# Kernel tuning notes

Measured on AMD Instinct MI355X. Metric: run time of the kernel, lower is better.

The kernel has to match this reference:

```python
import jax, jax.numpy as jnp
import numpy as np


def setup_inputs() -> dict:
    key = jax.random.key(0)
    kq, kk, kv = jax.random.split(key, 3)
    B, H, T, D = 2, 8, 8192, 64
    return {
        "Q": jax.random.normal(kq, (B, H, T, D), dtype=jnp.float32),
        "K": jax.random.normal(kk, (B, H, T, D), dtype=jnp.float32),
        "V": jax.random.normal(kv, (B, H, T, D), dtype=jnp.float32),
        "window_size": 512,
    }


def _gather_bands(x, nb, Wn):
    # x: [B,H,T,D] -> [B,H,nb,3*Wn,D], key blocks (i-1, i, i+1) per query block i
    B, H, T, D = x.shape
    xb = x.reshape(B, H, nb, Wn, D)
    xp = jnp.pad(xb, ((0, 0), (0, 0), (1, 1), (0, 0), (0, 0)))
    return jnp.concatenate([xp[:, :, i:i + nb] for i in range(3)], axis=3)


def reference(Q, K, V, window_size):
    # Sliding-window attention: softmax over keys with |q_idx - kv_idx| <= window_size,
    # computed block-sparsely (only the 3 neighboring key blocks per query block).
    B, H, T, D = Q.shape
    Wn = int(window_size)
    assert T % Wn == 0
    nb = T // Wn
    scale = 1.0 / (D ** 0.5)

    Qb = Q.reshape(B, H, nb, Wn, D)
    Kw = _gather_bands(K, nb, Wn)  # [B,H,nb,3W,D]
    Vw = _gather_bands(V, nb, Wn)

    # scores within the band: [B,H,nb,W,3W]
    s = jnp.einsum('bhnqd,bhnkd->bhnqk', Qb, Kw) * scale

    # exact band mask: global q = n*W + q_loc, global kv = (n-1)*W + k_loc
    q_loc = jnp.arange(Wn)[:, None]
    k_loc = jnp.arange(3 * Wn)[None, :]
    band = jnp.abs(q_loc + Wn - k_loc) <= Wn          # [W, 3W]
    kv_g = (jnp.arange(nb)[:, None] - 1) * Wn + jnp.arange(3 * Wn)[None, :]  # [nb, 3W]
    valid = (kv_g >= 0) & (kv_g < T)
    mask = band[None, :, :] & valid[:, None, :]        # [nb, W, 3W]

    s = jnp.where(mask[None, None], s, -jnp.inf)
    p = jax.nn.softmax(s, axis=-1)
    o = jnp.einsum('bhnqk,bhnkd->bhnqd', p, Vw)
    return o.reshape(B, H, T, D)
```

## Files before the change

### kernel.cpp

```cpp
#include <hip/hip_runtime.h>
#include <hip/hip_bf16.h>
#include <stdint.h>

typedef __attribute__((ext_vector_type(8))) short bf16x8;
typedef __attribute__((ext_vector_type(4))) short bf16x4;
typedef __attribute__((ext_vector_type(4))) float f32x4;

#define T_SEQ   8192
#define D_HEAD  64
#define NHEADS  16
#define WIN     512
#define BQ      128
#define BK      64
#define NTILES  (T_SEQ / BK)
#define LDSR    72
#define MASKVAL (-1.0e6f)

#define WS_NEEDED ((size_t)2 * NHEADS * T_SEQ * D_HEAD * 2)

#define MFMA16(a,b,c) __builtin_amdgcn_mfma_f32_16x16x16bf16_1k(a,b,c,0,0,0)

__device__ __forceinline__ short f2bf(float f) {
    union { float f; uint32_t u; } v; v.f = f;
    return (short)((v.u + 0x7FFFu + ((v.u >> 16) & 1u)) >> 16);
}

__device__ __forceinline__ uint32_t pkbf2(float lo, float hi) {
    union { __hip_bfloat162 h; uint32_t u; } c;
    c.h = __float22bfloat162_rn(make_float2(lo, hi));
    return c.u;
}

__global__ __launch_bounds__(256, 2)
void prep_kv(const float* __restrict__ Kg, const float* __restrict__ Vg,
             short* __restrict__ Kb, short* __restrict__ Vt)
{
    __shared__ float vt[64 * 65];
    const int tid  = threadIdx.x;
    const int tile = blockIdx.x & (NTILES - 1);
    const int head = blockIdx.x >> 7;
    const size_t off = ((size_t)head * T_SEQ + (size_t)tile * BK) * D_HEAD;

    const float* ks = Kg + off;
    short* kd = Kb + off;
    #pragma unroll
    for (int i = 0; i < 4; ++i) {
        int idx = tid + 256 * i;
        float4 v = *(const float4*)(ks + idx * 4);
        short4 h = { f2bf(v.x), f2bf(v.y), f2bf(v.z), f2bf(v.w) };
        *(short4*)(kd + idx * 4) = h;
    }

    const float* vs = Vg + off;
    #pragma unroll
    for (int i = 0; i < 4; ++i) {
        int idx = tid + 256 * i;
        int row = idx >> 4, c4 = (idx & 15) << 2;
        float4 v = *(const float4*)(vs + row * D_HEAD + c4);
        *(float4*)&vt[row * 65 + c4] = v;
    }
    __syncthreads();
    short* vd = Vt + ((size_t)head * NTILES + tile) * (BK * D_HEAD);
    {
        int d = tid >> 2, kq = (tid & 3) << 4;
        short out[16];
        #pragma unroll
        for (int j = 0; j < 16; ++j) out[j] = f2bf(vt[(kq + j) * 65 + d]);
        *(bf16x8*)(vd + d * BK + kq)     = *(bf16x8*)&out[0];
        *(bf16x8*)(vd + d * BK + kq + 8) = *(bf16x8*)&out[8];
    }
}

__global__ __launch_bounds__(256, 4)
void swa_fwd(const float* __restrict__ Qg, const short* __restrict__ Kb,
             const short* __restrict__ Vt, float* __restrict__ Og)
{
    __shared__ short Ks[BK * LDSR];
    __shared__ short Vs[D_HEAD * LDSR];

    const int tid  = threadIdx.x;
    const int wave = tid >> 6;
    const int lane = tid & 63;
    const int lcol = lane & 15;
    const int quad = lane >> 4;

    const int g    = blockIdx.x;
    const int head = (g >> 3) >> 3;
    const int qt   = ((g & 7) << 3) | ((g >> 3) & 7);
    const int q0   = qt * BQ;
    const int tq   = q0 >> 6;

    const float* Qp = Qg + (size_t)head * T_SEQ * D_HEAD;
    const short* Kp = Kb + (size_t)head * T_SEQ * D_HEAD;
    float*       Op = Og + (size_t)head * T_SEQ * D_HEAD;

    const float qscale = 0.125f * 1.44269504088896340736f;
    const int qrow_w = q0 + wave * 32;

    bf16x8 qf[2][2];
    #pragma unroll
    for (int mt = 0; mt < 2; ++mt) {
        const float* qptr = Qp + (size_t)(qrow_w + mt*16 + lcol) * D_HEAD + quad * 8;
        #pragma unroll
        for (int ks = 0; ks < 2; ++ks) {
            float4 a = *(const float4*)(qptr + ks*32);
            float4 b = *(const float4*)(qptr + ks*32 + 4);
            bf16x8 f;
            f[0]=f2bf(a.x*qscale); f[1]=f2bf(a.y*qscale); f[2]=f2bf(a.z*qscale); f[3]=f2bf(a.w*qscale);
            f[4]=f2bf(b.x*qscale); f[5]=f2bf(b.y*qscale); f[6]=f2bf(b.z*qscale); f[7]=f2bf(b.w*qscale);
            qf[mt][ks] = f;
        }
    }

    f32x4 oacc[2][4];
    float l_run[2];
    const f32x4 zero4 = {0.f, 0.f, 0.f, 0.f};
    #pragma unroll
    for (int mt = 0; mt < 2; ++mt) {
        l_run[mt] = 0.f;
        #pragma unroll
        for (int nt = 0; nt < 4; ++nt) oacc[mt][nt] = zero4;
    }

    int t0 = (q0 - WIN) >> 6;            if (t0 < 0) t0 = 0;
    int t1 = (q0 + BQ - 1 + WIN) >> 6;   if (t1 > NTILES - 1) t1 = NTILES - 1;

    for (int t = t0; t <= t1; ++t) {
        __syncthreads();
        {
            const short* ksrc = Kp + (size_t)t * BK * D_HEAD;
            const short* vsrc = Vt + ((size_t)head * NTILES + t) * (BK * D_HEAD);
            #pragma unroll
            for (int i = 0; i < 2; ++i) {
                int idx = tid + 256 * i;
                int row = idx >> 3, c = (idx & 7) << 3;
                *(bf16x8*)&Ks[row * LDSR + c] = *(const bf16x8*)(ksrc + idx * 8);
                *(bf16x8*)&Vs[row * LDSR + c] = *(const bf16x8*)(vsrc + idx * 8);
            }
        }
        __syncthreads();

        const bool edge = (t < tq - 6) || (t > tq + 7);

        #pragma unroll
        for (int h = 0; h < 2; ++h) {
            f32x4 sc[2][2];
            #pragma unroll
            for (int j = 0; j < 2; ++j) { sc[j][0] = zero4; sc[j][1] = zero4; }
            #pragma unroll
            for (int ks = 0; ks < 2; ++ks) {
                #pragma unroll
                for (int j = 0; j < 2; ++j) {
                    bf16x8 kf = *(const bf16x8*)&Ks[((2*h+j)*16 + lcol)*LDSR + ks*32 + quad*8];
                    sc[j][0] = __builtin_amdgcn_mfma_f32_16x16x32_bf16(kf, qf[0][ks], sc[j][0], 0,0,0);
                    sc[j][1] = __builtin_amdgcn_mfma_f32_16x16x32_bf16(kf, qf[1][ks], sc[j][1], 0,0,0);
                }
            }

            if (edge) {
                #pragma unroll
                for (int j = 0; j < 2; ++j) {
                    const int kg0 = t*BK + (2*h+j)*16 + quad*4;
                    #pragma unroll
                    for (int mt = 0; mt < 2; ++mt) {
                        const int qg = qrow_w + mt*16 + lcol;
                        #pragma unroll
                        for (int r = 0; r < 4; ++r) {
                            int dq = qg - (kg0 + r);
                            if (dq > WIN || dq < -WIN) sc[j][mt][r] = MASKVAL;
                        }
                    }
                }
            }

            #pragma unroll
            for (int j = 0; j < 2; ++j) {
                const int kt = 2*h + j;
                bf16x4 vf[4];
                #pragma unroll
                for (int nt = 0; nt < 4; ++nt)
                    vf[nt] = *(const bf16x4*)&Vs[(nt*16 + lcol)*LDSR + kt*16 + quad*4];
                #pragma unroll
                for (int mt = 0; mt < 2; ++mt) {
                    float p0 = exp2f(sc[j][mt][0]);
                    float p1 = exp2f(sc[j][mt][1]);
                    float p2 = exp2f(sc[j][mt][2]);
                    float p3 = exp2f(sc[j][mt][3]);
                    l_run[mt] += (p0 + p1) + (p2 + p3);
                    union { int2 i; bf16x4 v; } pf;
                    pf.i = make_int2((int)pkbf2(p0, p1), (int)pkbf2(p2, p3));
                    #pragma unroll
                    for (int nt = 0; nt < 4; ++nt)
                        oacc[mt][nt] = MFMA16(vf[nt], pf.v, oacc[mt][nt]);
                }
            }
        }
    }

    #pragma unroll
    for (int mt = 0; mt < 2; ++mt) {
        float l = l_run[mt];
        l += __shfl_xor(l, 16, 64);
        l += __shfl_xor(l, 32, 64);
        float inv = 1.0f / l;
        const int qg = qrow_w + mt*16 + lcol;
        float* op = Op + (size_t)qg * D_HEAD + quad*4;
        #pragma unroll
        for (int nt = 0; nt < 4; ++nt) {
            float4 o = { oacc[mt][nt][0]*inv, oacc[mt][nt][1]*inv,
                         oacc[mt][nt][2]*inv, oacc[mt][nt][3]*inv };
            *(float4*)(op + nt*16) = o;
        }
    }
}

#define M_INIT  (-1.0e4f)
__global__ __launch_bounds__(256, 2)
void swa_fwd_fb(const float* __restrict__ Qg, const float* __restrict__ Kg,
                const float* __restrict__ Vg, float* __restrict__ Og)
{
    __shared__ short Ks[BK * LDSR];
    __shared__ short Vs[D_HEAD * LDSR];
    __shared__ short Ps[4 * 32 * LDSR];

    const int tid  = threadIdx.x;
    const int wave = tid >> 6;
    const int lane = tid & 63;
    const int lcol = lane & 15;
    const int quad = lane >> 4;

    const int g    = blockIdx.x;
    const int head = (g >> 3) >> 3;
    const int qt   = ((g & 7) << 3) | ((g >> 3) & 7);
    const int q0   = qt * BQ;

    const size_t base = (size_t)head * T_SEQ * D_HEAD;
    const float* Qp = Qg + base;
    const float* Kp = Kg + base;
    const float* Vp = Vg + base;
    float*       Op = Og + base;

    const float qscale = 0.125f * 1.44269504088896340736f;
    const int qrow_w = q0 + wave * 32;

    bf16x8 qf[2][2];
    #pragma unroll
    for (int mt = 0; mt < 2; ++mt) {
        const float* qptr = Qp + (size_t)(qrow_w + mt*16 + lcol) * D_HEAD + quad * 8;
        #pragma unroll
        for (int ks = 0; ks < 2; ++ks) {
            float4 a = *(const float4*)(qptr + ks*32);
            float4 b = *(const float4*)(qptr + ks*32 + 4);
            bf16x8 f;
            f[0]=f2bf(a.x*qscale); f[1]=f2bf(a.y*qscale); f[2]=f2bf(a.z*qscale); f[3]=f2bf(a.w*qscale);
            f[4]=f2bf(b.x*qscale); f[5]=f2bf(b.y*qscale); f[6]=f2bf(b.z*qscale); f[7]=f2bf(b.w*qscale);
            qf[mt][ks] = f;
        }
    }

    f32x4 oacc[2][4];
    float m_run[2][4], l_run[2][4];
    const f32x4 zero4 = {0.f, 0.f, 0.f, 0.f};
    #pragma unroll
    for (int mt = 0; mt < 2; ++mt) {
        #pragma unroll
        for (int r = 0; r < 4; ++r) { m_run[mt][r] = M_INIT; l_run[mt][r] = 0.f; }
        #pragma unroll
        for (int nt = 0; nt < 4; ++nt) oacc[mt][nt] = zero4;
    }

    int t0 = (q0 - WIN) >> 6;            if (t0 < 0) t0 = 0;
    int t1 = (q0 + BQ - 1 + WIN) >> 6;   if (t1 > NTILES - 1) t1 = NTILES - 1;

    for (int t = t0; t <= t1; ++t) {
        __syncthreads();
        {
            const float* src = Kp + (size_t)t * BK * D_HEAD;
            #pragma unroll
            for (int i = 0; i < 4; ++i) {
                int f4 = tid + 256*i;
                int row = f4 >> 4, c4 = (f4 & 15) << 2;
                float4 v = *(const float4*)(src + row*D_HEAD + c4);
                short4 h = { f2bf(v.x), f2bf(v.y), f2bf(v.z), f2bf(v.w) };
                *(short4*)&Ks[row*LDSR + c4] = h;
            }
            const float* vsrc = Vp + (size_t)t * BK * D_HEAD;
            int col = tid & 63, rb = (tid >> 6) << 2;
            #pragma unroll
            for (int i = 0; i < 4; ++i) {
                int r = rb + 16*i;
                short4 h = { f2bf(vsrc[(r+0)*D_HEAD + col]),
                             f2bf(vsrc[(r+1)*D_HEAD + col]),
                             f2bf(vsrc[(r+2)*D_HEAD + col]),
                             f2bf(vsrc[(r+3)*D_HEAD + col]) };
                *(short4*)&Vs[col*LDSR + r] = h;
            }
        }
        __syncthreads();

        f32x4 sc[2][4];
        #pragma unroll
        for (int mt = 0; mt < 2; ++mt)
            #pragma unroll
            for (int kt = 0; kt < 4; ++kt) sc[mt][kt] = zero4;
        #pragma unroll
        for (int kt = 0; kt < 4; ++kt) {
            #pragma unroll
            for (int ks = 0; ks < 2; ++ks) {
                bf16x8 kf = *(const bf16x8*)&Ks[(kt*16 + lcol)*LDSR + ks*32 + quad*8];
                sc[0][kt] = __builtin_amdgcn_mfma_f32_16x16x32_bf16(qf[0][ks], kf, sc[0][kt], 0,0,0);
                sc[1][kt] = __builtin_amdgcn_mfma_f32_16x16x32_bf16(qf[1][ks], kf, sc[1][kt], 0,0,0);
            }
        }

        const int kb = t * BK + lcol;
        #pragma unroll
        for (int mt = 0; mt < 2; ++mt) {
            const int qrow = qrow_w + mt*16 + quad*4;
            #pragma unroll
            for (int kt = 0; kt < 4; ++kt) {
                int kg = kb + kt*16;
                #pragma unroll
                for (int r = 0; r < 4; ++r) {
                    int dq = (qrow + r) - kg;
                    if (dq > WIN || dq < -WIN) sc[mt][kt][r] = MASKVAL;
                }
            }
            float tm[4], al[4], rs[4];
            #pragma unroll
            for (int r = 0; r < 4; ++r)
                tm[r] = fmaxf(fmaxf(sc[mt][0][r], sc[mt][1][r]), fmaxf(sc[mt][2][r], sc[mt][3][r]));
            #pragma unroll
            for (int off = 1; off < 16; off <<= 1)
                #pragma unroll
                for (int r = 0; r < 4; ++r)
                    tm[r] = fmaxf(tm[r], __shfl_xor(tm[r], off, 64));
            #pragma unroll
            for (int r = 0; r < 4; ++r) {
                float mn = fmaxf(m_run[mt][r], tm[r]);
                al[r] = exp2f(m_run[mt][r] - mn);
                m_run[mt][r] = mn;
                rs[r] = 0.f;
            }
            #pragma unroll
            for (int kt = 0; kt < 4; ++kt)
                #pragma unroll
                for (int r = 0; r < 4; ++r) {
                    float p = exp2f(sc[mt][kt][r] - m_run[mt][r]);
                    sc[mt][kt][r] = p;
                    rs[r] += p;
                }
            #pragma unroll
            for (int off = 1; off < 16; off <<= 1)
                #pragma unroll
                for (int r = 0; r < 4; ++r)
                    rs[r] += __shfl_xor(rs[r], off, 64);
            #pragma unroll
            for (int r = 0; r < 4; ++r)
                l_run[mt][r] = l_run[mt][r]*al[r] + rs[r];
            #pragma unroll
            for (int nt = 0; nt < 4; ++nt)
                #pragma unroll
                for (int r = 0; r < 4; ++r) oacc[mt][nt][r] *= al[r];
            short* pw = &Ps[(wave*32 + mt*16 + quad*4) * LDSR];
            #pragma unroll
            for (int kt = 0; kt < 4; ++kt)
                #pragma unroll
                for (int r = 0; r < 4; ++r)
                    pw[r*LDSR + kt*16 + lcol] = f2bf(sc[mt][kt][r]);
        }

        const short* pr = &Ps[wave*32*LDSR];
        #pragma unroll
        for (int ks = 0; ks < 2; ++ks) {
            bf16x8 pf0 = *(const bf16x8*)&pr[(lcol     )*LDSR + ks*32 + quad*8];
            bf16x8 pf1 = *(const bf16x8*)&pr[(16 + lcol)*LDSR + ks*32 + quad*8];
            #pragma unroll
            for (int nt = 0; nt < 4; ++nt) {
                bf16x8 vf = *(const bf16x8*)&Vs[(nt*16 + lcol)*LDSR + ks*32 + quad*8];
                oacc[0][nt] = __builtin_amdgcn_mfma_f32_16x16x32_bf16(pf0, vf, oacc[0][nt], 0,0,0);
                oacc[1][nt] = __builtin_amdgcn_mfma_f32_16x16x32_bf16(pf1, vf, oacc[1][nt], 0,0,0);
            }
        }
    }

    #pragma unroll
    for (int mt = 0; mt < 2; ++mt)
        #pragma unroll
        for (int r = 0; r < 4; ++r) {
            int row = qrow_w + mt*16 + quad*4 + r;
            float inv = 1.0f / l_run[mt][r];
            float* op = Op + (size_t)row * D_HEAD + lcol;
            #pragma unroll
            for (int nt = 0; nt < 4; ++nt)
                op[nt*16] = oacc[mt][nt][r] * inv;
        }
}

extern "C" void kernel_launch(void* const* d_in, const int* in_sizes, int n_in,
                              void* d_out, int out_size, void* d_ws, size_t ws_size,
                              hipStream_t stream)
{
    const float* Q = (const float*)d_in[0];
    const float* K = (const float*)d_in[1];
    const float* V = (const float*)d_in[2];
    float* O = (float*)d_out;

    if (ws_size >= WS_NEEDED) {
        short* Kb = (short*)d_ws;
        short* Vt = Kb + (size_t)NHEADS * T_SEQ * D_HEAD;
        prep_kv<<<dim3(NHEADS * NTILES), dim3(256), 0, stream>>>(K, V, Kb, Vt);
        swa_fwd<<<dim3(NHEADS * (T_SEQ / BQ)), dim3(256), 0, stream>>>(Q, Kb, Vt, O);
    } else {
        swa_fwd_fb<<<dim3(NHEADS * (T_SEQ / BQ)), dim3(256), 0, stream>>>(Q, K, V, O);
    }
}
```

Before: 199.5 us.

## Double-buffer fragment-ordered KV tiles with larger query blocks and wider MFMA

The prep kernel now writes K and transposed V for each tile in one buffer, already in MFMA fragment order, so tiles can be copied into LDS without padding and read with aligned vector loads. The main kernel doubles the query block to 256 rows, so each wave handles 64 queries and K/V reuse per load goes up. It prefetches the next tile into registers while computing on the current one, using a ping-pong LDS buffer with one barrier per tile. The P·V product now uses 16x16x32 MFMAs instead of 16x16x16, and a wave skips tiles outside its own window. The costs are higher register pressure (occupancy hint drops from 4 to 2 blocks per CU) and half as many blocks.

```diff
diff --git a/kernel.cpp b/kernel.cpp
--- a/kernel.cpp
+++ b/kernel.cpp
@@ -10,15 +10,16 @@
 #define D_HEAD  64
 #define NHEADS  16
 #define WIN     512
-#define BQ      128
+#define BQ      256
 #define BK      64
-#define NTILES  (T_SEQ / BK)
-#define LDSR    72
+#define NTILES  128
+#define NQT     32
+#define TILE_SH 8192
 #define MASKVAL (-1.0e6f)
 
-#define WS_NEEDED ((size_t)2 * NHEADS * T_SEQ * D_HEAD * 2)
-
-#define MFMA16(a,b,c) __builtin_amdgcn_mfma_f32_16x16x16bf16_1k(a,b,c,0,0,0)
+#define WS_NEEDED ((size_t)NHEADS * NTILES * TILE_SH * sizeof(short))
+
+#define MFMA32(a,b,c) __builtin_amdgcn_mfma_f32_16x16x32_bf16(a,b,c,0,0,0)
 
 __device__ __forceinline__ short f2bf(float f) {
     union { float f; uint32_t u; } v; v.f = f;
@@ -33,50 +34,58 @@
 
 __global__ __launch_bounds__(256, 2)
 void prep_kv(const float* __restrict__ Kg, const float* __restrict__ Vg,
-             short* __restrict__ Kb, short* __restrict__ Vt)
+             short* __restrict__ KVf)
 {
     __shared__ float vt[64 * 65];
     const int tid  = threadIdx.x;
     const int tile = blockIdx.x & (NTILES - 1);
     const int head = blockIdx.x >> 7;
     const size_t off = ((size_t)head * T_SEQ + (size_t)tile * BK) * D_HEAD;
-
-    const float* ks = Kg + off;
-    short* kd = Kb + off;
-    #pragma unroll
-    for (int i = 0; i < 4; ++i) {
-        int idx = tid + 256 * i;
-        float4 v = *(const float4*)(ks + idx * 4);
-        short4 h = { f2bf(v.x), f2bf(v.y), f2bf(v.z), f2bf(v.w) };
-        *(short4*)(kd + idx * 4) = h;
-    }
+    short* KV = KVf + ((size_t)head * NTILES + tile) * TILE_SH;
 
     const float* vs = Vg + off;
     #pragma unroll
     for (int i = 0; i < 4; ++i) {
         int idx = tid + 256 * i;
         int row = idx >> 4, c4 = (idx & 15) << 2;
-        float4 v = *(const float4*)(vs + row * D_HEAD + c4);
-        *(float4*)&vt[row * 65 + c4] = v;
-    }
+        *(float4*)&vt[row * 65 + c4] = *(const float4*)(vs + row * D_HEAD + c4);
+    }
+
+    const float* ksrc = Kg + off;
+    #pragma unroll
+    for (int i = 0; i < 2; ++i) {
+        int b = tid + 256 * i;
+        int quad = b & 3, key = (b >> 2) & 15, ks = (b >> 6) & 1, kc = b >> 7;
+        const float* src = ksrc + (kc * 16 + key) * D_HEAD + ks * 32 + quad * 8;
+        float4 a = *(const float4*)src;
+        float4 c = *(const float4*)(src + 4);
+        bf16x8 o;
+        o[0]=f2bf(a.x); o[1]=f2bf(a.y); o[2]=f2bf(a.z); o[3]=f2bf(a.w);
+        o[4]=f2bf(c.x); o[5]=f2bf(c.y); o[6]=f2bf(c.z); o[7]=f2bf(c.w);
+        *(bf16x8*)(KV + b * 8) = o;
+    }
+
     __syncthreads();
-    short* vd = Vt + ((size_t)head * NTILES + tile) * (BK * D_HEAD);
-    {
-        int d = tid >> 2, kq = (tid & 3) << 4;
-        short out[16];
-        #pragma unroll
-        for (int j = 0; j < 16; ++j) out[j] = f2bf(vt[(kq + j) * 65 + d]);
-        *(bf16x8*)(vd + d * BK + kq)     = *(bf16x8*)&out[0];
-        *(bf16x8*)(vd + d * BK + kq + 8) = *(bf16x8*)&out[8];
-    }
-}
-
-__global__ __launch_bounds__(256, 4)
-void swa_fwd(const float* __restrict__ Qg, const short* __restrict__ Kb,
-             const short* __restrict__ Vt, float* __restrict__ Og)
+
+    #pragma unroll
+    for (int i = 0; i < 2; ++i) {
+        int b = tid + 256 * i;
+        int quad = b & 3, dl = (b >> 2) & 15, nt = (b >> 6) & 3, h = b >> 8;
+        int col = nt * 16 + dl;
+        bf16x8 o;
+        #pragma unroll
+        for (int j = 0; j < 4; ++j) o[j]     = f2bf(vt[(h*32 +      quad*4 + j) * 65 + col]);
+        #pragma unroll
+        for (int j = 0; j < 4; ++j) o[4 + j] = f2bf(vt[(h*32 + 16 + quad*4 + j) * 65 + col]);
+        *(bf16x8*)(KV + 4096 + b * 8) = o;
+    }
+}
+
+__global__ __launch_bounds__(256, 2)
+void swa_fwd(const float* __restrict__ Qg, const short* __restrict__ KVf,
+             float* __restrict__ Og)
 {
-    __shared__ short Ks[BK * LDSR];
-    __shared__ short Vs[D_HEAD * LDSR];
+    __shared__ __align__(16) short Buf[2][TILE_SH];
 
     const int tid  = threadIdx.x;
     const int wave = tid >> 6;
@@ -85,21 +94,21 @@
     const int quad = lane >> 4;
 
     const int g    = blockIdx.x;
-    const int head = (g >> 3) >> 3;
-    const int qt   = ((g & 7) << 3) | ((g >> 3) & 7);
+    const int head = ((g & 7) << 1) | ((g >> 3) & 1);
+    const int qt   = g >> 4;
     const int q0   = qt * BQ;
-    const int tq   = q0 >> 6;
-
-    const float* Qp = Qg + (size_t)head * T_SEQ * D_HEAD;
-    const short* Kp = Kb + (size_t)head * T_SEQ * D_HEAD;
-    float*       Op = Og + (size_t)head * T_SEQ * D_HEAD;
+    const int tb   = qt * 4;
+
+    const float* Qp  = Qg  + (size_t)head * T_SEQ * D_HEAD;
+    float*       Op  = Og  + (size_t)head * T_SEQ * D_HEAD;
+    const short* KVh = KVf + (size_t)head * NTILES * TILE_SH;
 
     const float qscale = 0.125f * 1.44269504088896340736f;
-    const int qrow_w = q0 + wave * 32;
-
-    bf16x8 qf[2][2];
-    #pragma unroll
-    for (int mt = 0; mt < 2; ++mt) {
+    const int qrow_w = q0 + wave * 64;
+
+    bf16x8 qf[4][2];
+    #pragma unroll
+    for (int mt = 0; mt < 4; ++mt) {
         const float* qptr = Qp + (size_t)(qrow_w + mt*16 + lcol) * D_HEAD + quad * 8;
         #pragma unroll
         for (int ks = 0; ks < 2; ++ks) {
@@ -112,93 +121,108 @@
         }
     }
 
-    f32x4 oacc[2][4];
-    float l_run[2];
+    f32x4 oacc[4][4];
+    float l_run[4];
     const f32x4 zero4 = {0.f, 0.f, 0.f, 0.f};
     #pragma unroll
-    for (int mt = 0; mt < 2; ++mt) {
+    for (int mt = 0; mt < 4; ++mt) {
         l_run[mt] = 0.f;
         #pragma unroll
         for (int nt = 0; nt < 4; ++nt) oacc[mt][nt] = zero4;
     }
 
-    int t0 = (q0 - WIN) >> 6;            if (t0 < 0) t0 = 0;
-    int t1 = (q0 + BQ - 1 + WIN) >> 6;   if (t1 > NTILES - 1) t1 = NTILES - 1;
-
+    int t0 = tb - 8;  if (t0 < 0) t0 = 0;
+    int t1 = tb + 11; if (t1 > NTILES - 1) t1 = NTILES - 1;
+
+    {
+        const short* src = KVh + (size_t)t0 * TILE_SH + tid * 8;
+        #pragma unroll
+        for (int i = 0; i < 4; ++i)
+            *(bf16x8*)&Buf[0][tid*8 + i*2048] = *(const bf16x8*)(src + i*2048);
+    }
+    __syncthreads();
+
+    int cur = 0;
     for (int t = t0; t <= t1; ++t) {
-        __syncthreads();
-        {
-            const short* ksrc = Kp + (size_t)t * BK * D_HEAD;
-            const short* vsrc = Vt + ((size_t)head * NTILES + t) * (BK * D_HEAD);
-            #pragma unroll
-            for (int i = 0; i < 2; ++i) {
-                int idx = tid + 256 * i;
-                int row = idx >> 3, c = (idx & 7) << 3;
-                *(bf16x8*)&Ks[row * LDSR + c] = *(const bf16x8*)(ksrc + idx * 8);
-                *(bf16x8*)&Vs[row * LDSR + c] = *(const bf16x8*)(vsrc + idx * 8);
-            }
-        }
-        __syncthreads();
-
-        const bool edge = (t < tq - 6) || (t > tq + 7);
-
-        #pragma unroll
-        for (int h = 0; h < 2; ++h) {
-            f32x4 sc[2][2];
-            #pragma unroll
-            for (int j = 0; j < 2; ++j) { sc[j][0] = zero4; sc[j][1] = zero4; }
-            #pragma unroll
-            for (int ks = 0; ks < 2; ++ks) {
-                #pragma unroll
-                for (int j = 0; j < 2; ++j) {
-                    bf16x8 kf = *(const bf16x8*)&Ks[((2*h+j)*16 + lcol)*LDSR + ks*32 + quad*8];
-                    sc[j][0] = __builtin_amdgcn_mfma_f32_16x16x32_bf16(kf, qf[0][ks], sc[j][0], 0,0,0);
-                    sc[j][1] = __builtin_amdgcn_mfma_f32_16x16x32_bf16(kf, qf[1][ks], sc[j][1], 0,0,0);
-                }
-            }
-
-            if (edge) {
-                #pragma unroll
-                for (int j = 0; j < 2; ++j) {
-                    const int kg0 = t*BK + (2*h+j)*16 + quad*4;
+        bf16x8 pre[4];
+        const bool have = (t < t1);
+        if (have) {
+            const short* src = KVh + (size_t)(t + 1) * TILE_SH + tid * 8;
+            #pragma unroll
+            for (int i = 0; i < 4; ++i) pre[i] = *(const bf16x8*)(src + i*2048);
+        }
+
+        if (t*BK <= qrow_w + 63 + WIN && t*BK + 63 >= qrow_w - WIN) {
+            const short* Kl = Buf[cur];
+            const short* Vl = Buf[cur] + 4096;
+            const bool edge = (t < tb - 4) || (t > tb + 7);
+
+            #pragma unroll
+            for (int h = 0; h < 2; ++h) {
+                bf16x4 pq[2][4];
+                #pragma unroll
+                for (int jj = 0; jj < 2; ++jj) {
+                    const int kc = h*2 + jj;
+                    bf16x8 kf0 = *(const bf16x8*)&Kl[((kc*2 + 0)*64 + lcol*4 + quad) * 8];
+                    bf16x8 kf1 = *(const bf16x8*)&Kl[((kc*2 + 1)*64 + lcol*4 + quad) * 8];
+                    f32x4 sc[4];
                     #pragma unroll
-                    for (int mt = 0; mt < 2; ++mt) {
-                        const int qg = qrow_w + mt*16 + lcol;
+                    for (int mt = 0; mt < 4; ++mt) sc[mt] = zero4;
+                    #pragma unroll
+                    for (int mt = 0; mt < 4; ++mt) {
+                        sc[mt] = MFMA32(kf0, qf[mt][0], sc[mt]);
+                        sc[mt] = MFMA32(kf1, qf[mt][1], sc[mt]);
+                    }
+                    if (edge) {
+                        const int kg0 = t*BK + kc*16 + quad*4;
                         #pragma unroll
-                        for (int r = 0; r < 4; ++r) {
-                            int dq = qg - (kg0 + r);
-                            if (dq > WIN || dq < -WIN) sc[j][mt][r] = MASKVAL;
+                        for (int mt = 0; mt < 4; ++mt) {
+                            const int qg = qrow_w + mt*16 + lcol;
+                            #pragma unroll
+                            for (int r = 0; r < 4; ++r) {
+                                int dq = qg - (kg0 + r);
+                                if (dq > WIN || dq < -WIN) sc[mt][r] = MASKVAL;
+                            }
                         }
                     }
+                    #pragma unroll
+                    for (int mt = 0; mt < 4; ++mt) {
+                        float p0 = exp2f(sc[mt][0]), p1 = exp2f(sc[mt][1]);
+                        float p2 = exp2f(sc[mt][2]), p3 = exp2f(sc[mt][3]);
+                        l_run[mt] += (p0 + p1) + (p2 + p3);
+                        union { int2 i2; bf16x4 v; } u;
+                        u.i2 = make_int2((int)pkbf2(p0, p1), (int)pkbf2(p2, p3));
+                        pq[jj][mt] = u.v;
+                    }
                 }
-            }
-
-            #pragma unroll
-            for (int j = 0; j < 2; ++j) {
-                const int kt = 2*h + j;
-                bf16x4 vf[4];
-                #pragma unroll
-                for (int nt = 0; nt < 4; ++nt)
-                    vf[nt] = *(const bf16x4*)&Vs[(nt*16 + lcol)*LDSR + kt*16 + quad*4];
-                #pragma unroll
-                for (int mt = 0; mt < 2; ++mt) {
-                    float p0 = exp2f(sc[j][mt][0]);
-                    float p1 = exp2f(sc[j][mt][1]);
-                    float p2 = exp2f(sc[j][mt][2]);
-                    float p3 = exp2f(sc[j][mt][3]);
-                    l_run[mt] += (p0 + p1) + (p2 + p3);
-                    union { int2 i; bf16x4 v; } pf;
-                    pf.i = make_int2((int)pkbf2(p0, p1), (int)pkbf2(p2, p3));
+                bf16x8 pf[4];
+                #pragma unroll
+                for (int mt = 0; mt < 4; ++mt) {
+                    union { bf16x8 v; bf16x4 q[2]; } u;
+                    u.q[0] = pq[0][mt]; u.q[1] = pq[1][mt];
+                    pf[mt] = u.v;
+                }
+                #pragma unroll
+                for (int nt = 0; nt < 4; ++nt) {
+                    bf16x8 vf = *(const bf16x8*)&Vl[((h*4 + nt)*64 + lcol*4 + quad) * 8];
                     #pragma unroll
-                    for (int nt = 0; nt < 4; ++nt)
-                        oacc[mt][nt] = MFMA16(vf[nt], pf.v, oacc[mt][nt]);
+                    for (int mt = 0; mt < 4; ++mt)
+                        oacc[mt][nt] = MFMA32(vf, pf[mt], oacc[mt][nt]);
                 }
             }
         }
-    }
-
-    #pragma unroll
-    for (int mt = 0; mt < 2; ++mt) {
+
+        if (have) {
+            #pragma unroll
+            for (int i = 0; i < 4; ++i)
+                *(bf16x8*)&Buf[cur ^ 1][tid*8 + i*2048] = pre[i];
+        }
+        __syncthreads();
+        cur ^= 1;
+    }
+
+    #pragma unroll
+    for (int mt = 0; mt < 4; ++mt) {
         float l = l_run[mt];
         l += __shfl_xor(l, 16, 64);
         l += __shfl_xor(l, 32, 64);
@@ -214,6 +238,7 @@
     }
 }
 
+#define LDSR    72
 #define M_INIT  (-1.0e4f)
 __global__ __launch_bounds__(256, 2)
 void swa_fwd_fb(const float* __restrict__ Qg, const float* __restrict__ Kg,
@@ -232,7 +257,7 @@
     const int g    = blockIdx.x;
     const int head = (g >> 3) >> 3;
     const int qt   = ((g & 7) << 3) | ((g >> 3) & 7);
-    const int q0   = qt * BQ;
+    const int q0   = qt * 128;
 
     const size_t base = (size_t)head * T_SEQ * D_HEAD;
     const float* Qp = Qg + base;
@@ -270,7 +295,7 @@
     }
 
     int t0 = (q0 - WIN) >> 6;            if (t0 < 0) t0 = 0;
-    int t1 = (q0 + BQ - 1 + WIN) >> 6;   if (t1 > NTILES - 1) t1 = NTILES - 1;
+    int t1 = (q0 + 127 + WIN) >> 6;      if (t1 > NTILES - 1) t1 = NTILES - 1;
 
     for (int t = t0; t <= t1; ++t) {
         __syncthreads();
@@ -281,19 +306,19 @@
                 int f4 = tid + 256*i;
                 int row = f4 >> 4, c4 = (f4 & 15) << 2;
                 float4 v = *(const float4*)(src + row*D_HEAD + c4);
-                short4 h = { f2bf(v.x), f2bf(v.y), f2bf(v.z), f2bf(v.w) };
-                *(short4*)&Ks[row*LDSR + c4] = h;
+                short4 hh = { f2bf(v.x), f2bf(v.y), f2bf(v.z), f2bf(v.w) };
+                *(short4*)&Ks[row*LDSR + c4] = hh;
             }
             const float* vsrc = Vp + (size_t)t * BK * D_HEAD;
             int col = tid & 63, rb = (tid >> 6) << 2;
             #pragma unroll
             for (int i = 0; i < 4; ++i) {
                 int r = rb + 16*i;
-                short4 h = { f2bf(vsrc[(r+0)*D_HEAD + col]),
-                             f2bf(vsrc[(r+1)*D_HEAD + col]),
-                             f2bf(vsrc[(r+2)*D_HEAD + col]),
-                             f2bf(vsrc[(r+3)*D_HEAD + col]) };
-                *(short4*)&Vs[col*LDSR + r] = h;
+                short4 hh = { f2bf(vsrc[(r+0)*D_HEAD + col]),
+                              f2bf(vsrc[(r+1)*D_HEAD + col]),
+                              f2bf(vsrc[(r+2)*D_HEAD + col]),
+                              f2bf(vsrc[(r+3)*D_HEAD + col]) };
+                *(short4*)&Vs[col*LDSR + r] = hh;
             }
         }
         __syncthreads();
@@ -308,8 +333,8 @@
             #pragma unroll
             for (int ks = 0; ks < 2; ++ks) {
                 bf16x8 kf = *(const bf16x8*)&Ks[(kt*16 + lcol)*LDSR + ks*32 + quad*8];
-                sc[0][kt] = __builtin_amdgcn_mfma_f32_16x16x32_bf16(qf[0][ks], kf, sc[0][kt], 0,0,0);
-                sc[1][kt] = __builtin_amdgcn_mfma_f32_16x16x32_bf16(qf[1][ks], kf, sc[1][kt], 0,0,0);
+                sc[0][kt] = MFMA32(qf[0][ks], kf, sc[0][kt]);
+                sc[1][kt] = MFMA32(qf[1][ks], kf, sc[1][kt]);
             }
         }
 
@@ -378,8 +403,8 @@
             #pragma unroll
             for (int nt = 0; nt < 4; ++nt) {
                 bf16x8 vf = *(const bf16x8*)&Vs[(nt*16 + lcol)*LDSR + ks*32 + quad*8];
-                oacc[0][nt] = __builtin_amdgcn_mfma_f32_16x16x32_bf16(pf0, vf, oacc[0][nt], 0,0,0);
-                oacc[1][nt] = __builtin_amdgcn_mfma_f32_16x16x32_bf16(pf1, vf, oacc[1][nt], 0,0,0);
+                oacc[0][nt] = MFMA32(pf0, vf, oacc[0][nt]);
+                oacc[1][nt] = MFMA32(pf1, vf, oacc[1][nt]);
             }
         }
     }
@@ -407,11 +432,10 @@
     float* O = (float*)d_out;
 
     if (ws_size >= WS_NEEDED) {
-        short* Kb = (short*)d_ws;
-        short* Vt = Kb + (size_t)NHEADS * T_SEQ * D_HEAD;
-        prep_kv<<<dim3(NHEADS * NTILES), dim3(256), 0, stream>>>(K, V, Kb, Vt);
-        swa_fwd<<<dim3(NHEADS * (T_SEQ / BQ)), dim3(256), 0, stream>>>(Q, Kb, Vt, O);
+        short* KVf = (short*)d_ws;
+        prep_kv<<<dim3(NHEADS * NTILES), dim3(256), 0, stream>>>(K, V, KVf);
+        swa_fwd<<<dim3(NHEADS * NQT), dim3(256), 0, stream>>>(Q, KVf, O);
     } else {
-        swa_fwd_fb<<<dim3(NHEADS * (T_SEQ / BQ)), dim3(256), 0, stream>>>(Q, K, V, O);
-    }
-}
+        swa_fwd_fb<<<dim3(NHEADS * 64), dim3(256), 0, stream>>>(Q, K, V, O);
+    }
+}
```

Result: slower. 205.5 us (+3.0%).
